# Performance work log

Measured on AMD Instinct MI355X. Metric: run time of the kernel, lower is better.

The kernel has to match this reference:

```python
import jax, jax.numpy as jnp
import numpy as np
from jax import lax

INPUT = 99
HIDDEN = 64
T = 65536


def setup_inputs() -> dict:
    key = jax.random.key(0)
    ks = jax.random.split(key, 8)
    x = jax.random.normal(ks[0], (1, T, INPUT), dtype=jnp.float32)
    # PyTorch LSTM params: weight_ih_l0 [4H, in], weight_hh_l0 [4H, H], biases [4H]
    s = 1.0 / np.sqrt(HIDDEN)
    W_ih = jax.random.uniform(ks[1], (4 * HIDDEN, INPUT), jnp.float32, -s, s)
    W_hh = jax.random.uniform(ks[2], (4 * HIDDEN, HIDDEN), jnp.float32, -s, s)
    b_ih = jax.random.uniform(ks[3], (4 * HIDDEN,), jnp.float32, -s, s)
    b_hh = jax.random.uniform(ks[4], (4 * HIDDEN,), jnp.float32, -s, s)
    # head: Linear(64->32, bias=False), Linear(32->3, bias=True)
    W1 = jax.random.normal(ks[5], (32, HIDDEN), dtype=jnp.float32) * 0.01
    W2 = jax.random.normal(ks[6], (3, 32), dtype=jnp.float32) * 0.01
    b2 = jnp.zeros((3,), dtype=jnp.float32)
    return {"x": x, "W_ih": W_ih, "W_hh": W_hh, "b_ih": b_ih, "b_hh": b_hh,
            "W1": W1, "W2": W2, "b2": b2}


def reference(x, W_ih, W_hh, b_ih, b_hh, W1, W2, b2):
    H = HIDDEN
    # Precompute input projections for all timesteps (one big GEMM).
    # x: [1, T, 99] -> xz: [T, 4H]; x[-1] == last (only) batch row.
    xz = jnp.einsum('td,gd->tg', x[-1], W_ih) + b_ih + b_hh

    def step(carry, z_t):
        h, c = carry
        z = z_t + W_hh @ h  # [4H]
        i, f, g, o = jnp.split(z, 4)  # PyTorch gate order: i, f, g, o
        i = jax.nn.sigmoid(i)
        f = jax.nn.sigmoid(f)
        g = jnp.tanh(g)
        o = jax.nn.sigmoid(o)
        c = f * c + i * g
        h = o * jnp.tanh(c)
        return (h, c), None

    h0 = jnp.zeros((H,), dtype=x.dtype)
    c0 = jnp.zeros((H,), dtype=x.dtype)
    (h_T, _), _ = lax.scan(step, (h0, c0), xz)

    # x[-1, -1] -> last timestep hidden of last batch row, then MLP head
    h = jax.nn.relu(h_T)
    h = jax.nn.relu(W1 @ h)
    out = W2 @ h + b2
    return out[None, :]  # [1, 3]
```

## Files before the change

kernel.cpp:

```cpp
#include <hip/hip_runtime.h>

#define T_STEPS 65536
#define NIN 99
#define HID 64
#define G4 256
#define TS 128
#define PF 8

__device__ __forceinline__ float frcp(float x) { return __builtin_amdgcn_rcpf(x); }
__device__ __forceinline__ float fexp(float x) { return __expf(x); }
__device__ __forceinline__ float sigmoid_f(float x) { return frcp(1.0f + fexp(-x)); }
__device__ __forceinline__ float tanh_f(float x) {
    float ax = fabsf(x);
    float e  = fexp(2.0f * ax);
    float r  = 1.0f - 2.0f * frcp(e + 1.0f);
    return copysignf(r, x);
}
__device__ __forceinline__ float bcast(float v, int lane) {
    return __int_as_float(__builtin_amdgcn_readlane(__float_as_int(v), lane));
}

#define BAR_LGKM() asm volatile("s_waitcnt lgkmcnt(0)\n\ts_barrier" ::: "memory")

__global__ __launch_bounds__(256, 1) void xz_kernel(
    const float* __restrict__ x, const float* __restrict__ W_ih,
    const float* __restrict__ b_ih, const float* __restrict__ b_hh,
    float* __restrict__ xz2) {
    __shared__ __align__(16) float xs[TS * 100];
    const int g  = threadIdx.x;
    const int t0 = blockIdx.x * TS;
    const int unit = g & 63, d = g >> 6;

    for (int i = g; i < TS * NIN; i += 256) {
        int tl = i / NIN;
        int j  = i - tl * NIN;
        xs[tl * 100 + j] = x[(size_t)t0 * NIN + i];
    }

    float w[NIN];
#pragma unroll
    for (int j = 0; j < NIN; ++j) w[j] = W_ih[g * NIN + j];
    const float bias = b_ih[g] + b_hh[g];
    __syncthreads();

    for (int tl = 0; tl < TS; ++tl) {
        const float* xr = &xs[tl * 100];
        float a0 = bias, a1 = 0.f, a2 = 0.f, a3 = 0.f;
#pragma unroll
        for (int j4 = 0; j4 < 24; ++j4) {
            float4 xv = *(const float4*)(xr + 4 * j4);
            a0 = fmaf(w[4 * j4 + 0], xv.x, a0);
            a1 = fmaf(w[4 * j4 + 1], xv.y, a1);
            a2 = fmaf(w[4 * j4 + 2], xv.z, a2);
            a3 = fmaf(w[4 * j4 + 3], xv.w, a3);
        }
        a0 = fmaf(w[96], xr[96], a0);
        a1 = fmaf(w[97], xr[97], a1);
        a2 = fmaf(w[98], xr[98], a2);
        xz2[(size_t)(t0 + tl) * G4 + unit * 4 + d] = (a0 + a1) + (a2 + a3);
    }
}

__global__ __launch_bounds__(256, 1) __attribute__((amdgpu_waves_per_eu(1)))
void lstm_kernel(
    const float* __restrict__ xz2, const float* __restrict__ W_hh,
    const float* __restrict__ W1, const float* __restrict__ W2,
    const float* __restrict__ b2, float* __restrict__ out) {
    __shared__ __align__(16) float4 pbuf[2][4][HID];
    __shared__ float hfin[HID];
    __shared__ float hbuf[32];
    const int tid = threadIdx.x;
    const int l   = tid & 63;
    const int wv  = tid >> 6;
    const int sb  = __builtin_amdgcn_readfirstlane(16 * wv);

    const float* Wb = W_hh + l * HID + sb;
    float4 wi0 = *(const float4*)(Wb +     0), wi1 = *(const float4*)(Wb +     4),
           wi2 = *(const float4*)(Wb +     8), wi3 = *(const float4*)(Wb +    12);
    float4 wf0 = *(const float4*)(Wb +  4096), wf1 = *(const float4*)(Wb +  4100),
           wf2 = *(const float4*)(Wb +  4104), wf3 = *(const float4*)(Wb +  4108);
    float4 wg0 = *(const float4*)(Wb +  8192), wg1 = *(const float4*)(Wb +  8196),
           wg2 = *(const float4*)(Wb +  8200), wg3 = *(const float4*)(Wb +  8204);
    float4 wo0 = *(const float4*)(Wb + 12288), wo1 = *(const float4*)(Wb + 12292),
           wo2 = *(const float4*)(Wb + 12296), wo3 = *(const float4*)(Wb + 12300);

#define PIN4(v) asm volatile("" : "+v"(v.x), "+v"(v.y), "+v"(v.z), "+v"(v.w))
    PIN4(wi0); PIN4(wi1); PIN4(wi2); PIN4(wi3);
    PIN4(wf0); PIN4(wf1); PIN4(wf2); PIN4(wf3);
    PIN4(wg0); PIN4(wg1); PIN4(wg2); PIN4(wg3);
    PIN4(wo0); PIN4(wo1); PIN4(wo2); PIN4(wo3);
#undef PIN4

    float h = 0.0f, c = 0.0f;

    const float* zi = xz2 + 4 * l;
    float4 zcur[PF], znxt[PF];
    if (wv == 0) {
#pragma unroll
        for (int p = 0; p < PF; ++p) zcur[p] = *(const float4*)(zi + (size_t)p * G4);
    }

#define STEP_J4(J4, WI, WF, WG, WO)                                             \
    {   float hx0 = bcast(h, sb + 4 * J4 + 0);                                  \
        float hx1 = bcast(h, sb + 4 * J4 + 1);                                  \
        float hx2 = bcast(h, sb + 4 * J4 + 2);                                  \
        float hx3 = bcast(h, sb + 4 * J4 + 3);                                  \
        ai = fmaf(WI.x, hx0, ai); ai = fmaf(WI.y, hx1, ai);                     \
        ai = fmaf(WI.z, hx2, ai); ai = fmaf(WI.w, hx3, ai);                     \
        af = fmaf(WF.x, hx0, af); af = fmaf(WF.y, hx1, af);                     \
        af = fmaf(WF.z, hx2, af); af = fmaf(WF.w, hx3, af);                     \
        ag = fmaf(WG.x, hx0, ag); ag = fmaf(WG.y, hx1, ag);                     \
        ag = fmaf(WG.z, hx2, ag); ag = fmaf(WG.w, hx3, ag);                     \
        ao = fmaf(WO.x, hx0, ao); ao = fmaf(WO.y, hx1, ao);                     \
        ao = fmaf(WO.z, hx2, ao); ao = fmaf(WO.w, hx3, ao); }

    for (int tb = 0; tb < T_STEPS; tb += PF) {
        if (wv == 0 && tb + PF < T_STEPS) {
#pragma unroll
            for (int p = 0; p < PF; ++p)
                znxt[p] = *(const float4*)(zi + (size_t)(tb + PF + p) * G4);
        }
#pragma unroll
        for (int u = 0; u < PF; ++u) {
            const int par = u & 1;
            float ai, af, ag, ao;
            if (wv == 0) { ai = zcur[u].x; af = zcur[u].y; ag = zcur[u].z; ao = zcur[u].w; }
            else         { ai = 0.f; af = 0.f; ag = 0.f; ao = 0.f; }
            STEP_J4(0, wi0, wf0, wg0, wo0)
            STEP_J4(1, wi1, wf1, wg1, wo1)
            STEP_J4(2, wi2, wf2, wg2, wo2)
            STEP_J4(3, wi3, wf3, wg3, wo3)
            pbuf[par][wv][l] = make_float4(ai, af, ag, ao);
            BAR_LGKM();

            float4 r0 = pbuf[par][(wv + 1) & 3][l];
            float4 r1 = pbuf[par][(wv + 2) & 3][l];
            float4 r2 = pbuf[par][(wv + 3) & 3][l];
            float si = (ai + r0.x) + (r1.x + r2.x);
            float sf = (af + r0.y) + (r1.y + r2.y);
            float sg = (ag + r0.z) + (r1.z + r2.z);
            float so = (ao + r0.w) + (r1.w + r2.w);
            float ig = sigmoid_f(si);
            float fg = sigmoid_f(sf);
            float gg = tanh_f(sg);
            float og = sigmoid_f(so);
            c = fmaf(fg, c, ig * gg);
            h = og * tanh_f(c);
        }
        if (wv == 0) {
#pragma unroll
            for (int p = 0; p < PF; ++p) zcur[p] = znxt[p];
        }
    }
#undef STEP_J4

    if (tid < HID) hfin[tid] = h;
    __syncthreads();
    if (tid < 32) {
        float s = 0.0f;
#pragma unroll
        for (int j = 0; j < HID; ++j) s += W1[tid * HID + j] * fmaxf(hfin[j], 0.0f);
        hbuf[tid] = fmaxf(s, 0.0f);
    }
    __syncthreads();
    if (tid < 3) {
        float s = b2[tid];
#pragma unroll
        for (int j = 0; j < 32; ++j) s += W2[tid * 32 + j] * hbuf[j];
        out[tid] = s;
    }
}

extern "C" void kernel_launch(void* const* d_in, const int* in_sizes, int n_in,
                              void* d_out, int out_size, void* d_ws, size_t ws_size,
                              hipStream_t stream) {
    const float* x   = (const float*)d_in[0];
    const float* Wih = (const float*)d_in[1];
    const float* Whh = (const float*)d_in[2];
    const float* bih = (const float*)d_in[3];
    const float* bhh = (const float*)d_in[4];
    const float* W1  = (const float*)d_in[5];
    const float* W2  = (const float*)d_in[6];
    const float* b2  = (const float*)d_in[7];
    float* out = (float*)d_out;
    float* xz2 = (float*)d_ws;

    xz_kernel<<<T_STEPS / TS, 256, 0, stream>>>(x, Wih, bih, bhh, xz2);
    lstm_kernel<<<1, 256, 0, stream>>>(xz2, Whh, W1, W2, b2, out);
}
```

Before: 22.91 ms.

## Use packed FMA dot products and per-step rolling prefetch of input projections

The recurrent dot product now uses two-wide vector FMAs (packed FP32 FMA) with split accumulators, which halves the FMA instruction count and shortens each serial chain. The input-projection value is no longer added by wave 0 at the start of the chain; every wave loads it and adds it after the cross-wave reduction. The 8-step double-buffered prefetch is replaced by a 4-deep rolling register prefetch, with one load issued per step. All four waves now issue global loads, which adds memory traffic and a vmcnt wait inside the serial loop.

```diff
diff --git a/kernel.cpp b/kernel.cpp
--- a/kernel.cpp
+++ b/kernel.cpp
@@ -5,7 +5,8 @@
 #define HID 64
 #define G4 256
 #define TS 128
-#define PF 8
+
+typedef __attribute__((ext_vector_type(2))) float f32x2;
 
 __device__ __forceinline__ float frcp(float x) { return __builtin_amdgcn_rcpf(x); }
 __device__ __forceinline__ float fexp(float x) { return __expf(x); }
@@ -94,65 +95,64 @@
     float h = 0.0f, c = 0.0f;
 
     const float* zi = xz2 + 4 * l;
-    float4 zcur[PF], znxt[PF];
-    if (wv == 0) {
-#pragma unroll
-        for (int p = 0; p < PF; ++p) zcur[p] = *(const float4*)(zi + (size_t)p * G4);
+    float4 zb0 = *(const float4*)(zi + 0 * G4);
+    float4 zb1 = *(const float4*)(zi + 1 * G4);
+    float4 zb2 = *(const float4*)(zi + 2 * G4);
+    float4 zb3 = *(const float4*)(zi + 3 * G4);
+
+#define F2XY(v) ((f32x2){v.x, v.y})
+#define F2ZW(v) ((f32x2){v.z, v.w})
+#define PAIR(KOFF, HI, WI2, WF2, WG2, WO2)                                      \
+    {   f32x2 h2;                                                               \
+        h2.x = bcast(h, sb + (KOFF));                                           \
+        h2.y = bcast(h, sb + (KOFF) + 1);                                       \
+        (void)(HI);                                                             \
+        ai = __builtin_elementwise_fma(WI2, h2, ai);                            \
+        af = __builtin_elementwise_fma(WF2, h2, af);                            \
+        ag = __builtin_elementwise_fma(WG2, h2, ag);                            \
+        ao = __builtin_elementwise_fma(WO2, h2, ao); }
+
+#define STEP(U, PAR, ZB)                                                        \
+    {   float4 zv = ZB;                                                         \
+        \
+        {   int sn = tb + (U) + 4; sn = sn < T_STEPS ? sn : T_STEPS - 1;        \
+            ZB = *(const float4*)(zi + (size_t)sn * G4); }                      \
+        f32x2 ai = {0.f, 0.f}, af = {0.f, 0.f}, ag = {0.f, 0.f}, ao = {0.f, 0.f};\
+        PAIR(0,  0, F2XY(wi0), F2XY(wf0), F2XY(wg0), F2XY(wo0))                 \
+        PAIR(2,  0, F2ZW(wi0), F2ZW(wf0), F2ZW(wg0), F2ZW(wo0))                 \
+        PAIR(4,  0, F2XY(wi1), F2XY(wf1), F2XY(wg1), F2XY(wo1))                 \
+        PAIR(6,  0, F2ZW(wi1), F2ZW(wf1), F2ZW(wg1), F2ZW(wo1))                 \
+        PAIR(8,  0, F2XY(wi2), F2XY(wf2), F2XY(wg2), F2XY(wo2))                 \
+        PAIR(10, 0, F2ZW(wi2), F2ZW(wf2), F2ZW(wg2), F2ZW(wo2))                 \
+        PAIR(12, 0, F2XY(wi3), F2XY(wf3), F2XY(wg3), F2XY(wo3))                 \
+        PAIR(14, 0, F2ZW(wi3), F2ZW(wf3), F2ZW(wg3), F2ZW(wo3))                 \
+        pbuf[PAR][wv][l] = make_float4(ai.x + ai.y, af.x + af.y,                \
+                                       ag.x + ag.y, ao.x + ao.y);               \
+        BAR_LGKM();                                                             \
+        float4 r0 = pbuf[PAR][(wv + 1) & 3][l];                                 \
+        float4 r1 = pbuf[PAR][(wv + 2) & 3][l];                                 \
+        float4 r2 = pbuf[PAR][(wv + 3) & 3][l];                                 \
+        float si = (zv.x + (ai.x + ai.y)) + ((r0.x + r1.x) + r2.x);             \
+        float sf = (zv.y + (af.x + af.y)) + ((r0.y + r1.y) + r2.y);             \
+        float sg = (zv.z + (ag.x + ag.y)) + ((r0.z + r1.z) + r2.z);             \
+        float so = (zv.w + (ao.x + ao.y)) + ((r0.w + r1.w) + r2.w);             \
+        float ig = sigmoid_f(si);                                               \
+        float fg = sigmoid_f(sf);                                               \
+        float gg = tanh_f(sg);                                                  \
+        float og = sigmoid_f(so);                                               \
+        c = fmaf(fg, c, ig * gg);                                               \
+        h = og * tanh_f(c); }
+
+    for (int tb = 0; tb < T_STEPS; tb += 4) {
+        STEP(0, 0, zb0)
+        STEP(1, 1, zb1)
+        STEP(2, 0, zb2)
+        STEP(3, 1, zb3)
     }
-
-#define STEP_J4(J4, WI, WF, WG, WO)                                             \
-    {   float hx0 = bcast(h, sb + 4 * J4 + 0);                                  \
-        float hx1 = bcast(h, sb + 4 * J4 + 1);                                  \
-        float hx2 = bcast(h, sb + 4 * J4 + 2);                                  \
-        float hx3 = bcast(h, sb + 4 * J4 + 3);                                  \
-        ai = fmaf(WI.x, hx0, ai); ai = fmaf(WI.y, hx1, ai);                     \
-        ai = fmaf(WI.z, hx2, ai); ai = fmaf(WI.w, hx3, ai);                     \
-        af = fmaf(WF.x, hx0, af); af = fmaf(WF.y, hx1, af);                     \
-        af = fmaf(WF.z, hx2, af); af = fmaf(WF.w, hx3, af);                     \
-        ag = fmaf(WG.x, hx0, ag); ag = fmaf(WG.y, hx1, ag);                     \
-        ag = fmaf(WG.z, hx2, ag); ag = fmaf(WG.w, hx3, ag);                     \
-        ao = fmaf(WO.x, hx0, ao); ao = fmaf(WO.y, hx1, ao);                     \
-        ao = fmaf(WO.z, hx2, ao); ao = fmaf(WO.w, hx3, ao); }
-
-    for (int tb = 0; tb < T_STEPS; tb += PF) {
-        if (wv == 0 && tb + PF < T_STEPS) {
-#pragma unroll
-            for (int p = 0; p < PF; ++p)
-                znxt[p] = *(const float4*)(zi + (size_t)(tb + PF + p) * G4);
-        }
-#pragma unroll
-        for (int u = 0; u < PF; ++u) {
-            const int par = u & 1;
-            float ai, af, ag, ao;
-            if (wv == 0) { ai = zcur[u].x; af = zcur[u].y; ag = zcur[u].z; ao = zcur[u].w; }
-            else         { ai = 0.f; af = 0.f; ag = 0.f; ao = 0.f; }
-            STEP_J4(0, wi0, wf0, wg0, wo0)
-            STEP_J4(1, wi1, wf1, wg1, wo1)
-            STEP_J4(2, wi2, wf2, wg2, wo2)
-            STEP_J4(3, wi3, wf3, wg3, wo3)
-            pbuf[par][wv][l] = make_float4(ai, af, ag, ao);
-            BAR_LGKM();
-
-            float4 r0 = pbuf[par][(wv + 1) & 3][l];
-            float4 r1 = pbuf[par][(wv + 2) & 3][l];
-            float4 r2 = pbuf[par][(wv + 3) & 3][l];
-            float si = (ai + r0.x) + (r1.x + r2.x);
-            float sf = (af + r0.y) + (r1.y + r2.y);
-            float sg = (ag + r0.z) + (r1.z + r2.z);
-            float so = (ao + r0.w) + (r1.w + r2.w);
-            float ig = sigmoid_f(si);
-            float fg = sigmoid_f(sf);
-            float gg = tanh_f(sg);
-            float og = sigmoid_f(so);
-            c = fmaf(fg, c, ig * gg);
-            h = og * tanh_f(c);
-        }
-        if (wv == 0) {
-#pragma unroll
-            for (int p = 0; p < PF; ++p) zcur[p] = znxt[p];
-        }
-    }
-#undef STEP_J4
+#undef STEP
+#undef PAIR
+#undef F2XY
+#undef F2ZW
 
     if (tid < HID) hfin[tid] = h;
     __syncthreads();
```

Result: slower. 23.90 ms (+4.3%).

## Split LSTM recurrence across two waves instead of four

Applied to the files above, without the earlier changes.

The recurrent kernel now runs with 128 threads (two wavefronts). Each wave covers 32 of the 64 hidden inputs, holding 128 weights in registers, and accumulates into two interleaved chains. The cross-wave reduction reads one partner buffer instead of three, and both waves load the precomputed input projection so it is added after the exchange. The goal is to cut barrier and LDS reduction cost per timestep, at the price of twice the serial FMA work per wave and higher register pressure.

```diff
diff --git a/kernel.cpp b/kernel.cpp
--- a/kernel.cpp
+++ b/kernel.cpp
@@ -5,7 +5,7 @@
 #define HID 64
 #define G4 256
 #define TS 128
-#define PF 8
+#define PF 4
 
 __device__ __forceinline__ float frcp(float x) { return __builtin_amdgcn_rcpf(x); }
 __device__ __forceinline__ float fexp(float x) { return __expf(x); }
@@ -61,61 +61,67 @@
     }
 }
 
-__global__ __launch_bounds__(256, 1) __attribute__((amdgpu_waves_per_eu(1)))
+__global__ __launch_bounds__(128, 1) __attribute__((amdgpu_waves_per_eu(1)))
 void lstm_kernel(
     const float* __restrict__ xz2, const float* __restrict__ W_hh,
     const float* __restrict__ W1, const float* __restrict__ W2,
     const float* __restrict__ b2, float* __restrict__ out) {
-    __shared__ __align__(16) float4 pbuf[2][4][HID];
+    __shared__ __align__(16) float4 pbuf[2][2][HID];
     __shared__ float hfin[HID];
     __shared__ float hbuf[32];
     const int tid = threadIdx.x;
     const int l   = tid & 63;
     const int wv  = tid >> 6;
-    const int sb  = __builtin_amdgcn_readfirstlane(16 * wv);
+    const int sb  = __builtin_amdgcn_readfirstlane(32 * wv);
 
     const float* Wb = W_hh + l * HID + sb;
-    float4 wi0 = *(const float4*)(Wb +     0), wi1 = *(const float4*)(Wb +     4),
-           wi2 = *(const float4*)(Wb +     8), wi3 = *(const float4*)(Wb +    12);
-    float4 wf0 = *(const float4*)(Wb +  4096), wf1 = *(const float4*)(Wb +  4100),
-           wf2 = *(const float4*)(Wb +  4104), wf3 = *(const float4*)(Wb +  4108);
-    float4 wg0 = *(const float4*)(Wb +  8192), wg1 = *(const float4*)(Wb +  8196),
-           wg2 = *(const float4*)(Wb +  8200), wg3 = *(const float4*)(Wb +  8204);
-    float4 wo0 = *(const float4*)(Wb + 12288), wo1 = *(const float4*)(Wb + 12292),
-           wo2 = *(const float4*)(Wb + 12296), wo3 = *(const float4*)(Wb + 12300);
+#define LD4(name, off) float4 name = *(const float4*)(Wb + (off))
+    LD4(wi0,     0); LD4(wi1,     4); LD4(wi2,     8); LD4(wi3,    12);
+    LD4(wi4,    16); LD4(wi5,    20); LD4(wi6,    24); LD4(wi7,    28);
+    LD4(wf0,  4096); LD4(wf1,  4100); LD4(wf2,  4104); LD4(wf3,  4108);
+    LD4(wf4,  4112); LD4(wf5,  4116); LD4(wf6,  4120); LD4(wf7,  4124);
+    LD4(wg0,  8192); LD4(wg1,  8196); LD4(wg2,  8200); LD4(wg3,  8204);
+    LD4(wg4,  8208); LD4(wg5,  8212); LD4(wg6,  8216); LD4(wg7,  8220);
+    LD4(wo0, 12288); LD4(wo1, 12292); LD4(wo2, 12296); LD4(wo3, 12300);
+    LD4(wo4, 12304); LD4(wo5, 12308); LD4(wo6, 12312); LD4(wo7, 12316);
+#undef LD4
 
 #define PIN4(v) asm volatile("" : "+v"(v.x), "+v"(v.y), "+v"(v.z), "+v"(v.w))
-    PIN4(wi0); PIN4(wi1); PIN4(wi2); PIN4(wi3);
-    PIN4(wf0); PIN4(wf1); PIN4(wf2); PIN4(wf3);
-    PIN4(wg0); PIN4(wg1); PIN4(wg2); PIN4(wg3);
-    PIN4(wo0); PIN4(wo1); PIN4(wo2); PIN4(wo3);
-#undef PIN4
+#define PIN_ALL()                                                   \
+    PIN4(wi0); PIN4(wi1); PIN4(wi2); PIN4(wi3);                     \
+    PIN4(wi4); PIN4(wi5); PIN4(wi6); PIN4(wi7);                     \
+    PIN4(wf0); PIN4(wf1); PIN4(wf2); PIN4(wf3);                     \
+    PIN4(wf4); PIN4(wf5); PIN4(wf6); PIN4(wf7);                     \
+    PIN4(wg0); PIN4(wg1); PIN4(wg2); PIN4(wg3);                     \
+    PIN4(wg4); PIN4(wg5); PIN4(wg6); PIN4(wg7);                     \
+    PIN4(wo0); PIN4(wo1); PIN4(wo2); PIN4(wo3);                     \
+    PIN4(wo4); PIN4(wo5); PIN4(wo6); PIN4(wo7)
+    PIN_ALL();
 
     float h = 0.0f, c = 0.0f;
 
     const float* zi = xz2 + 4 * l;
     float4 zcur[PF], znxt[PF];
-    if (wv == 0) {
 #pragma unroll
-        for (int p = 0; p < PF; ++p) zcur[p] = *(const float4*)(zi + (size_t)p * G4);
-    }
+    for (int p = 0; p < PF; ++p) zcur[p] = *(const float4*)(zi + (size_t)p * G4);
 
-#define STEP_J4(J4, WI, WF, WG, WO)                                             \
-    {   float hx0 = bcast(h, sb + 4 * J4 + 0);                                  \
-        float hx1 = bcast(h, sb + 4 * J4 + 1);                                  \
-        float hx2 = bcast(h, sb + 4 * J4 + 2);                                  \
-        float hx3 = bcast(h, sb + 4 * J4 + 3);                                  \
-        ai = fmaf(WI.x, hx0, ai); ai = fmaf(WI.y, hx1, ai);                     \
-        ai = fmaf(WI.z, hx2, ai); ai = fmaf(WI.w, hx3, ai);                     \
-        af = fmaf(WF.x, hx0, af); af = fmaf(WF.y, hx1, af);                     \
-        af = fmaf(WF.z, hx2, af); af = fmaf(WF.w, hx3, af);                     \
-        ag = fmaf(WG.x, hx0, ag); ag = fmaf(WG.y, hx1, ag);                     \
-        ag = fmaf(WG.z, hx2, ag); ag = fmaf(WG.w, hx3, ag);                     \
-        ao = fmaf(WO.x, hx0, ao); ao = fmaf(WO.y, hx1, ao);                     \
-        ao = fmaf(WO.z, hx2, ao); ao = fmaf(WO.w, hx3, ao); }
+#define QUAD(KOFF, WI, WF, WG, WO, AI, AF, AG, AO)                              \
+    {   float hx0 = bcast(h, sb + (KOFF) + 0);                                  \
+        float hx1 = bcast(h, sb + (KOFF) + 1);                                  \
+        float hx2 = bcast(h, sb + (KOFF) + 2);                                  \
+        float hx3 = bcast(h, sb + (KOFF) + 3);                                  \
+        AI = fmaf(WI.x, hx0, AI); AI = fmaf(WI.y, hx1, AI);                     \
+        AI = fmaf(WI.z, hx2, AI); AI = fmaf(WI.w, hx3, AI);                     \
+        AF = fmaf(WF.x, hx0, AF); AF = fmaf(WF.y, hx1, AF);                     \
+        AF = fmaf(WF.z, hx2, AF); AF = fmaf(WF.w, hx3, AF);                     \
+        AG = fmaf(WG.x, hx0, AG); AG = fmaf(WG.y, hx1, AG);                     \
+        AG = fmaf(WG.z, hx2, AG); AG = fmaf(WG.w, hx3, AG);                     \
+        AO = fmaf(WO.x, hx0, AO); AO = fmaf(WO.y, hx1, AO);                     \
+        AO = fmaf(WO.z, hx2, AO); AO = fmaf(WO.w, hx3, AO); }
 
     for (int tb = 0; tb < T_STEPS; tb += PF) {
-        if (wv == 0 && tb + PF < T_STEPS) {
+        PIN_ALL();
+        if (tb + PF < T_STEPS) {
 #pragma unroll
             for (int p = 0; p < PF; ++p)
                 znxt[p] = *(const float4*)(zi + (size_t)(tb + PF + p) * G4);
@@ -123,23 +129,26 @@
 #pragma unroll
         for (int u = 0; u < PF; ++u) {
             const int par = u & 1;
-            float ai, af, ag, ao;
-            if (wv == 0) { ai = zcur[u].x; af = zcur[u].y; ag = zcur[u].z; ao = zcur[u].w; }
-            else         { ai = 0.f; af = 0.f; ag = 0.f; ao = 0.f; }
-            STEP_J4(0, wi0, wf0, wg0, wo0)
-            STEP_J4(1, wi1, wf1, wg1, wo1)
-            STEP_J4(2, wi2, wf2, wg2, wo2)
-            STEP_J4(3, wi3, wf3, wg3, wo3)
+            float ai0 = 0.f, af0 = 0.f, ag0 = 0.f, ao0 = 0.f;
+            float ai1 = 0.f, af1 = 0.f, ag1 = 0.f, ao1 = 0.f;
+            QUAD( 0, wi0, wf0, wg0, wo0, ai0, af0, ag0, ao0)
+            QUAD( 4, wi1, wf1, wg1, wo1, ai1, af1, ag1, ao1)
+            QUAD( 8, wi2, wf2, wg2, wo2, ai0, af0, ag0, ao0)
+            QUAD(12, wi3, wf3, wg3, wo3, ai1, af1, ag1, ao1)
+            QUAD(16, wi4, wf4, wg4, wo4, ai0, af0, ag0, ao0)
+            QUAD(20, wi5, wf5, wg5, wo5, ai1, af1, ag1, ao1)
+            QUAD(24, wi6, wf6, wg6, wo6, ai0, af0, ag0, ao0)
+            QUAD(28, wi7, wf7, wg7, wo7, ai1, af1, ag1, ao1)
+            float ai = ai0 + ai1, af = af0 + af1, ag = ag0 + ag1, ao = ao0 + ao1;
             pbuf[par][wv][l] = make_float4(ai, af, ag, ao);
             BAR_LGKM();
 
-            float4 r0 = pbuf[par][(wv + 1) & 3][l];
-            float4 r1 = pbuf[par][(wv + 2) & 3][l];
-            float4 r2 = pbuf[par][(wv + 3) & 3][l];
-            float si = (ai + r0.x) + (r1.x + r2.x);
-            float sf = (af + r0.y) + (r1.y + r2.y);
-            float sg = (ag + r0.z) + (r1.z + r2.z);
-            float so = (ao + r0.w) + (r1.w + r2.w);
+            float4 r = pbuf[par][wv ^ 1][l];
+            float4 zv = zcur[u];
+            float si = (ai + r.x) + zv.x;
+            float sf = (af + r.y) + zv.y;
+            float sg = (ag + r.z) + zv.z;
+            float so = (ao + r.w) + zv.w;
             float ig = sigmoid_f(si);
             float fg = sigmoid_f(sf);
             float gg = tanh_f(sg);
@@ -147,12 +156,12 @@
             c = fmaf(fg, c, ig * gg);
             h = og * tanh_f(c);
         }
-        if (wv == 0) {
 #pragma unroll
-            for (int p = 0; p < PF; ++p) zcur[p] = znxt[p];
-        }
+        for (int p = 0; p < PF; ++p) zcur[p] = znxt[p];
     }
-#undef STEP_J4
+#undef QUAD
+#undef PIN_ALL
+#undef PIN4
 
     if (tid < HID) hfin[tid] = h;
     __syncthreads();
@@ -186,5 +195,5 @@
     float* xz2 = (float*)d_ws;
 
     xz_kernel<<<T_STEPS / TS, 256, 0, stream>>>(x, Wih, bih, bhh, xz2);
-    lstm_kernel<<<1, 256, 0, stream>>>(xz2, Whh, W1, W2, b2, out);
+    lstm_kernel<<<1, 128, 0, stream>>>(xz2, Whh, W1, W2, b2, out);
 }
```

Measured after the change: 27.68 ms. 1.21x slower.
